# Kernel optimization log

Hardware: AMD Instinct MI355X
Metric: run time of the kernel (lower is better)

The kernel has to match this reference:

```python
import jax, jax.numpy as jnp
import numpy as np

B, N, D, S, CD = 8, 2048, 512, 256, 768
H, DH = 8, 64
INNER = H * DH          # 512
FF = 4 * D              # 2048 (GEGLU inner)
EPS = 1e-5


def setup_inputs() -> dict:
    key = jax.random.key(0)
    ks = jax.random.split(key, 24)
    w = lambda k, shp: (jax.random.normal(k, shp, dtype=jnp.float32) * 0.02)
    inp = {
        "x": jax.random.normal(ks[0], (B, N, D), dtype=jnp.float32),
        "context": jax.random.normal(ks[1], (B, S, CD), dtype=jnp.float32),
        "lengths": jax.random.randint(ks[2], (B,), 1, N + 1).astype(jnp.int32),
        # self-attention (attn1)
        "wq1": w(ks[3], (D, INNER)), "wk1": w(ks[4], (D, INNER)), "wv1": w(ks[5], (D, INNER)),
        "wo1": w(ks[6], (INNER, D)), "bo1": jnp.zeros((D,), jnp.float32),
        # cross-attention (attn2)
        "wq2": w(ks[7], (D, INNER)), "wk2": w(ks[8], (CD, INNER)), "wv2": w(ks[9], (CD, INNER)),
        "wo2": w(ks[10], (INNER, D)), "bo2": jnp.zeros((D,), jnp.float32),
        # GEGLU feed-forward
        "wff_in": w(ks[11], (D, 2 * FF)), "bff_in": jnp.zeros((2 * FF,), jnp.float32),
        "wff_out": w(ks[12], (FF, D)), "bff_out": jnp.zeros((D,), jnp.float32),
        # LayerNorms
        "g1": jnp.ones((D,), jnp.float32), "b1": jnp.zeros((D,), jnp.float32),
        "g2": jnp.ones((D,), jnp.float32), "b2": jnp.zeros((D,), jnp.float32),
        "g3": jnp.ones((D,), jnp.float32), "b3": jnp.zeros((D,), jnp.float32),
    }
    return inp


def _ln(t, g, b):
    m = jnp.mean(t, axis=-1, keepdims=True)
    v = jnp.mean(jnp.square(t - m), axis=-1, keepdims=True)
    return (t - m) * jax.lax.rsqrt(v + EPS) * g + b


def _mha(q, k, v, key_mask):
    # q: [B,Nq,INNER], k/v: [B,Nk,INNER], key_mask: [B,Nk] bool or None
    split = lambda t: t.reshape(t.shape[0], t.shape[1], H, DH).transpose(0, 2, 1, 3)
    qh, kh, vh = split(q), split(k), split(v)
    scores = jnp.einsum("bhqd,bhkd->bhqk", qh, kh) * (DH ** -0.5)
    if key_mask is not None:
        scores = jnp.where(key_mask[:, None, None, :], scores, -1e30)
    attn = jax.nn.softmax(scores, axis=-1)
    out = jnp.einsum("bhqk,bhkd->bhqd", attn, vh)
    return out.transpose(0, 2, 1, 3).reshape(q.shape[0], q.shape[1], INNER)


def reference(x, context, lengths, wq1, wk1, wv1, wo1, bo1,
              wq2, wk2, wv2, wo2, bo2,
              wff_in, bff_in, wff_out, bff_out,
              g1, b1, g2, b2, g3, b3):
    tok_mask = jnp.arange(N)[None, :] < lengths[:, None]  # [B,N] valid tokens
    # --- self-attention (attn1), pre-norm, jagged -> key-masked ---
    h = _ln(x, g1, b1)
    a = _mha(h @ wq1, h @ wk1, h @ wv1, tok_mask) @ wo1 + bo1
    x = x + a
    # --- cross-attention (attn2) to dense context ---
    h = _ln(x, g2, b2)
    a = _mha(h @ wq2, context @ wk2, context @ wv2, None) @ wo2 + bo2
    x = x + a
    # --- GEGLU feed-forward ---
    h = _ln(x, g3, b3)
    p = h @ wff_in + bff_in
    a, gate = jnp.split(p, 2, axis=-1)
    x = x + (a * jax.nn.gelu(gate, approximate=False)) @ wff_out + bff_out
    # zero out padded positions (they don't exist in the jagged tensor)
    return x * tok_mask[..., None].astype(x.dtype)
```

## Files before the change

kernel.cpp:

```cpp
#include <hip/hip_runtime.h>
#include <stdint.h>


typedef __bf16 bf16x8 __attribute__((ext_vector_type(8)));
typedef float f32x4 __attribute__((ext_vector_type(4)));

__device__ __forceinline__ unsigned short f2b(float f) {
  union { float f; unsigned u; } v; v.f = f;
  return (unsigned short)((v.u + 0x7FFFu + ((v.u >> 16) & 1u)) >> 16);
}
__device__ __forceinline__ float b2f(unsigned short s) {
  union { unsigned u; float f; } v; v.u = ((unsigned)s) << 16; return v.f;
}
__device__ __forceinline__ f32x4 mfma16(bf16x8 a, bf16x8 b, f32x4 c) {
  return __builtin_amdgcn_mfma_f32_16x16x32_bf16(a, b, c, 0, 0, 0);
}

__global__ __launch_bounds__(256) void wtrans(const float* __restrict__ in,
                                              unsigned short* __restrict__ out,
                                              int R, int C) {
  __shared__ unsigned short t[32][33];
  int tx = threadIdx.x & 31, ty = threadIdx.x >> 5;
  int c0 = blockIdx.x * 32, r0 = blockIdx.y * 32;
#pragma unroll
  for (int i = 0; i < 32; i += 8)
    t[ty + i][tx] = f2b(in[(size_t)(r0 + ty + i) * C + c0 + tx]);
  __syncthreads();
#pragma unroll
  for (int i = 0; i < 32; i += 8)
    out[(size_t)(c0 + ty + i) * R + r0 + tx] = t[tx][ty + i];
}

__global__ __launch_bounds__(256) void castbf(const float* __restrict__ in,
                                              unsigned short* __restrict__ out,
                                              int n4) {
  int i = blockIdx.x * 256 + threadIdx.x;
  if (i >= n4) return;
  float4 v = ((const float4*)in)[i];
  unsigned long long p = (unsigned long long)f2b(v.x) |
                         ((unsigned long long)f2b(v.y) << 16) |
                         ((unsigned long long)f2b(v.z) << 32) |
                         ((unsigned long long)f2b(v.w) << 48);
  ((unsigned long long*)out)[i] = p;
}

__global__ __launch_bounds__(256) void ln_rows(const float* __restrict__ x,
                                               const float* __restrict__ g,
                                               const float* __restrict__ bb,
                                               unsigned short* __restrict__ out) {
  int row = blockIdx.x * 4 + (threadIdx.x >> 6);
  int lane = threadIdx.x & 63;
  const float* xr = x + (size_t)row * 512 + lane * 8;
  float4 a = *(const float4*)xr;
  float4 c = *(const float4*)(xr + 4);
  float av[8] = {a.x, a.y, a.z, a.w, c.x, c.y, c.z, c.w};
  float s = 0.f, q = 0.f;
#pragma unroll
  for (int j = 0; j < 8; j++) { s += av[j]; q += av[j] * av[j]; }
#pragma unroll
  for (int d = 1; d < 64; d <<= 1) { s += __shfl_xor(s, d); q += __shfl_xor(q, d); }
  float mean = s * (1.f / 512.f);
  float var = q * (1.f / 512.f) - mean * mean;
  float rs = rsqrtf(var + 1e-5f);
  const float* gp = g + lane * 8;
  const float* bp = bb + lane * 8;
  unsigned rr[4];
#pragma unroll
  for (int j = 0; j < 4; j++) {
    float y0 = (av[2 * j] - mean) * rs * gp[2 * j] + bp[2 * j];
    float y1 = (av[2 * j + 1] - mean) * rs * gp[2 * j + 1] + bp[2 * j + 1];
    rr[j] = (unsigned)f2b(y0) | ((unsigned)f2b(y1) << 16);
  }
  *(uint4*)(out + (size_t)row * 512 + lane * 8) = make_uint4(rr[0], rr[1], rr[2], rr[3]);
}

template <int EPI>
__global__ __launch_bounds__(256) void gemm128(const unsigned short* __restrict__ A,
                                               const unsigned short* __restrict__ Bt,
                                               void* __restrict__ Cp,
                                               const float* __restrict__ bias,
                                               const float* __restrict__ res,
                                               int M, int N, int K) {
  __shared__ unsigned short As[128 * 32];
  __shared__ unsigned short Bs[128 * 32];
  int tid = threadIdx.x;
  int wave = tid >> 6, lane = tid & 63;
  int row0 = blockIdx.x * 128, col0 = blockIdx.y * 128;
  int wr = wave >> 1, wc = wave & 1;
  f32x4 acc[4][4] = {};
  int sr = tid >> 1, sk = (tid & 1) << 4;
  const unsigned short* gA = A + (size_t)(row0 + sr) * K + sk;
  const unsigned short* gB = Bt + (size_t)(col0 + sr) * K + sk;
  int l15 = lane & 15, l4 = (lane >> 4) << 3;
  int rA = (wr * 64 + l15) * 32 + l4;
  int rB = (wc * 64 + l15) * 32 + l4;
  for (int kt = 0; kt < K; kt += 32) {
    *(uint4*)&As[sr * 32 + sk] = *(const uint4*)(gA + kt);
    *(uint4*)&As[sr * 32 + sk + 8] = *(const uint4*)(gA + kt + 8);
    *(uint4*)&Bs[sr * 32 + sk] = *(const uint4*)(gB + kt);
    *(uint4*)&Bs[sr * 32 + sk + 8] = *(const uint4*)(gB + kt + 8);
    __syncthreads();
    bf16x8 af[4], bq[4];
#pragma unroll
    for (int m = 0; m < 4; m++) af[m] = *(const bf16x8*)&As[rA + m * 16 * 32];
#pragma unroll
    for (int n = 0; n < 4; n++) bq[n] = *(const bf16x8*)&Bs[rB + n * 16 * 32];
#pragma unroll
    for (int m = 0; m < 4; m++)
#pragma unroll
      for (int n = 0; n < 4; n++)
        acc[m][n] = mfma16(af[m], bq[n], acc[m][n]);
    __syncthreads();
  }
  int lr = (lane >> 4) * 4;
#pragma unroll
  for (int m = 0; m < 4; m++)
#pragma unroll
    for (int n = 0; n < 4; n++)
#pragma unroll
      for (int r = 0; r < 4; r++) {
        int grow = row0 + wr * 64 + m * 16 + lr + r;
        int gcol = col0 + wc * 64 + n * 16 + l15;
        size_t gi = (size_t)grow * N + gcol;
        float v = acc[m][n][r];
        if (EPI == 0) {
          ((unsigned short*)Cp)[gi] = f2b(v);
        } else if (EPI == 1) {
          ((unsigned short*)Cp)[gi] = f2b(v + bias[gcol]);
        } else {
          ((float*)Cp)[gi] = v + bias[gcol] + res[gi];
        }
      }
}

__global__ __launch_bounds__(256) void attn(const unsigned short* __restrict__ Q,
                                            const unsigned short* __restrict__ Kg,
                                            const unsigned short* __restrict__ Vg,
                                            unsigned short* __restrict__ O,
                                            const int* __restrict__ lengths,
                                            int nq, int nkv, int maskkv) {
  int qblk = blockIdx.x, h = blockIdx.y, b = blockIdx.z;
  int tid = threadIdx.x, wave = tid >> 6, lane = tid & 63;
  int len = lengths[b];
  int qbase = qblk * 64;
  if (qbase >= len) return;
  int kvlen = maskkv ? len : nkv;
  int nt = (kvlen + 31) >> 5;

  __shared__ unsigned short Ks[32][72];
  __shared__ unsigned short Vf[2048];
  __shared__ unsigned short Ps[4][16][40];

  int l15 = lane & 15, lh = lane >> 4, l4 = lh * 8;
  const unsigned short* qp =
      Q + (size_t)(b * nq + qbase + wave * 16 + l15) * 512 + h * 64 + l4;
  bf16x8 aq0 = *(const bf16x8*)qp;
  bf16x8 aq1 = *(const bf16x8*)(qp + 32);
  const unsigned short* kgp = Kg + (size_t)b * nkv * 512 + h * 64;
  const unsigned short* vgp = Vg + (size_t)b * nkv * 512 + h * 64;

  f32x4 oacc[4] = {};
  float m_r[4], l_r[4];
#pragma unroll
  for (int r = 0; r < 4; r++) { m_r[r] = -3e38f; l_r[r] = 0.f; }

  int skey = tid >> 3, sd0 = (tid & 7) * 8;
  int vdh = tid & 63, vkg = tid >> 6;

  for (int t = 0; t < nt; t++) {
    int kv0 = t * 32;
    *(uint4*)&Ks[skey][sd0] =
        *(const uint4*)(kgp + (size_t)(kv0 + skey) * 512 + sd0);
    {
      unsigned short tmp[8];
#pragma unroll
      for (int kj = 0; kj < 8; kj++)
        tmp[kj] = vgp[(size_t)(kv0 + vkg * 8 + kj) * 512 + vdh];
      unsigned w0 = (unsigned)tmp[0] | ((unsigned)tmp[1] << 16);
      unsigned w1 = (unsigned)tmp[2] | ((unsigned)tmp[3] << 16);
      unsigned w2 = (unsigned)tmp[4] | ((unsigned)tmp[5] << 16);
      unsigned w3 = (unsigned)tmp[6] | ((unsigned)tmp[7] << 16);
      *(uint4*)&Vf[(vkg * 64 + vdh) * 8] = make_uint4(w0, w1, w2, w3);
    }
    __syncthreads();

    f32x4 sf[2];
#pragma unroll
    for (int c = 0; c < 2; c++) {
      bf16x8 bk0 = *(const bf16x8*)&Ks[c * 16 + l15][l4];
      bf16x8 bk1 = *(const bf16x8*)&Ks[c * 16 + l15][32 + l4];
      f32x4 z = {};
      z = mfma16(aq0, bk0, z);
      z = mfma16(aq1, bk1, z);
      sf[c] = z;
    }
#pragma unroll
    for (int c = 0; c < 2; c++) {
      bool kval = (kv0 + c * 16 + l15) < kvlen;
#pragma unroll
      for (int r = 0; r < 4; r++)
        sf[c][r] = kval ? sf[c][r] * 0.125f : -1e30f;
    }
    float mt[4], ps[4];
#pragma unroll
    for (int r = 0; r < 4; r++) mt[r] = fmaxf(sf[0][r], sf[1][r]);
#pragma unroll
    for (int d = 1; d < 16; d <<= 1)
#pragma unroll
      for (int r = 0; r < 4; r++) mt[r] = fmaxf(mt[r], __shfl_xor(mt[r], d));
    float sc[4];
#pragma unroll
    for (int r = 0; r < 4; r++) {
      float mn = fmaxf(m_r[r], mt[r]);
      sc[r] = __expf(m_r[r] - mn);
      m_r[r] = mn;
      ps[r] = 0.f;
    }
#pragma unroll
    for (int c = 0; c < 2; c++)
#pragma unroll
      for (int r = 0; r < 4; r++) {
        float pe = __expf(sf[c][r] - m_r[r]);
        ps[r] += pe;
        Ps[wave][lh * 4 + r][c * 16 + l15] = f2b(pe);
      }
#pragma unroll
    for (int d = 1; d < 16; d <<= 1)
#pragma unroll
      for (int r = 0; r < 4; r++) ps[r] += __shfl_xor(ps[r], d);
#pragma unroll
    for (int r = 0; r < 4; r++) l_r[r] = l_r[r] * sc[r] + ps[r];
#pragma unroll
    for (int nf = 0; nf < 4; nf++)
#pragma unroll
      for (int r = 0; r < 4; r++) oacc[nf][r] *= sc[r];
    bf16x8 pf = *(const bf16x8*)&Ps[wave][l15][l4];
#pragma unroll
    for (int nf = 0; nf < 4; nf++) {
      bf16x8 vf = *(const bf16x8*)&Vf[(lh * 64 + nf * 16 + l15) * 8];
      oacc[nf] = mfma16(pf, vf, oacc[nf]);
    }
    __syncthreads();
  }
#pragma unroll
  for (int nf = 0; nf < 4; nf++)
#pragma unroll
    for (int r = 0; r < 4; r++) {
      float ov = oacc[nf][r] / l_r[r];
      int qrow = qbase + wave * 16 + lh * 4 + r;
      O[(size_t)(b * nq + qrow) * 512 + h * 64 + nf * 16 + l15] = f2b(ov);
    }
}

__global__ __launch_bounds__(256) void geglu(const unsigned short* __restrict__ p,
                                             unsigned short* __restrict__ out) {
  int idx = blockIdx.x * 256 + threadIdx.x;
  int row = idx >> 8, c = (idx & 255) << 3;
  const unsigned short* pr = p + (size_t)row * 4096 + c;
  uint4 av = *(const uint4*)pr;
  uint4 gv = *(const uint4*)(pr + 2048);
  const unsigned short* ap = (const unsigned short*)&av;
  const unsigned short* gp = (const unsigned short*)&gv;
  unsigned rr[4];
#pragma unroll
  for (int j = 0; j < 4; j++) {
    float a0 = b2f(ap[2 * j]), a1 = b2f(ap[2 * j + 1]);
    float x0 = b2f(gp[2 * j]), x1 = b2f(gp[2 * j + 1]);
    float y0 = a0 * 0.5f * x0 * (1.f + erff(x0 * 0.70710678118f));
    float y1 = a1 * 0.5f * x1 * (1.f + erff(x1 * 0.70710678118f));
    rr[j] = (unsigned)f2b(y0) | ((unsigned)f2b(y1) << 16);
  }
  *(uint4*)(out + (size_t)row * 2048 + c) = make_uint4(rr[0], rr[1], rr[2], rr[3]);
}

__global__ __launch_bounds__(256) void maskout_f32(const float* __restrict__ xb,
                                                   const int* __restrict__ lengths,
                                                   float* __restrict__ out) {
  int idx = blockIdx.x * 256 + threadIdx.x;
  int row = idx >> 6, c = (idx & 63) << 3;
  int b = row >> 11, n = row & 2047;
  bool val = n < lengths[b];
  float4 v0 = make_float4(0.f, 0.f, 0.f, 0.f), v1 = v0;
  if (val) {
    const float* xr = xb + (size_t)row * 512 + c;
    v0 = *(const float4*)xr;
    v1 = *(const float4*)(xr + 4);
  }
  float* orp = out + (size_t)row * 512 + c;
  *(float4*)orp = v0;
  *(float4*)(orp + 4) = v1;
}

extern "C" void kernel_launch(void* const* d_in, const int* in_sizes, int n_in,
                              void* d_out, int out_size, void* d_ws, size_t ws_size,
                              hipStream_t stream) {
  const float* x = (const float*)d_in[0];
  const float* ctx = (const float*)d_in[1];
  const int* lengths = (const int*)d_in[2];
  const float* wq1 = (const float*)d_in[3];
  const float* wk1 = (const float*)d_in[4];
  const float* wv1 = (const float*)d_in[5];
  const float* wo1 = (const float*)d_in[6];
  const float* bo1 = (const float*)d_in[7];
  const float* wq2 = (const float*)d_in[8];
  const float* wk2 = (const float*)d_in[9];
  const float* wv2 = (const float*)d_in[10];
  const float* wo2 = (const float*)d_in[11];
  const float* bo2 = (const float*)d_in[12];
  const float* wffin = (const float*)d_in[13];
  const float* bffin = (const float*)d_in[14];
  const float* wffout = (const float*)d_in[15];
  const float* bffout = (const float*)d_in[16];
  const float* g1 = (const float*)d_in[17];
  const float* b1 = (const float*)d_in[18];
  const float* g2 = (const float*)d_in[19];
  const float* b2 = (const float*)d_in[20];
  const float* g3 = (const float*)d_in[21];
  const float* b3 = (const float*)d_in[22];

  char* ws = (char*)d_ws;
  size_t o = 0;
  auto alloc = [&](size_t bytes) {
    size_t r = o;
    o += (bytes + 255) & ~(size_t)255;
    return r;
  };
  unsigned short* WQ1T = (unsigned short*)(ws + alloc(512 * 512 * 2));
  unsigned short* WK1T = (unsigned short*)(ws + alloc(512 * 512 * 2));
  unsigned short* WV1T = (unsigned short*)(ws + alloc(512 * 512 * 2));
  unsigned short* WO1T = (unsigned short*)(ws + alloc(512 * 512 * 2));
  unsigned short* WQ2T = (unsigned short*)(ws + alloc(512 * 512 * 2));
  unsigned short* WK2T = (unsigned short*)(ws + alloc(512 * 768 * 2));
  unsigned short* WV2T = (unsigned short*)(ws + alloc(512 * 768 * 2));
  unsigned short* WO2T = (unsigned short*)(ws + alloc(512 * 512 * 2));
  unsigned short* WFFINT = (unsigned short*)(ws + alloc(4096 * 512 * 2));
  unsigned short* WFFOUTT = (unsigned short*)(ws + alloc(512 * 2048 * 2));
  float* XBUF = (float*)(ws + alloc((size_t)16384 * 512 * 4));
  unsigned short* HB = (unsigned short*)(ws + alloc((size_t)16384 * 512 * 2));
  unsigned short* QB = (unsigned short*)(ws + alloc((size_t)16384 * 512 * 2));
  unsigned short* KB = (unsigned short*)(ws + alloc((size_t)16384 * 512 * 2));
  unsigned short* VB = (unsigned short*)(ws + alloc((size_t)16384 * 512 * 2));
  unsigned short* AO = (unsigned short*)(ws + alloc((size_t)16384 * 512 * 2));
  unsigned short* CTXB = KB;
  unsigned short* K2B = KB + (size_t)4 * 1024 * 1024 / 2;
  unsigned short* V2B = KB + (size_t)8 * 1024 * 1024 / 2;
  unsigned short* PCH = QB;
  unsigned short* GCH = VB;

  wtrans<<<dim3(16, 16), 256, 0, stream>>>(wq1, WQ1T, 512, 512);
  wtrans<<<dim3(16, 16), 256, 0, stream>>>(wk1, WK1T, 512, 512);
  wtrans<<<dim3(16, 16), 256, 0, stream>>>(wv1, WV1T, 512, 512);
  wtrans<<<dim3(16, 16), 256, 0, stream>>>(wo1, WO1T, 512, 512);
  wtrans<<<dim3(16, 16), 256, 0, stream>>>(wq2, WQ2T, 512, 512);
  wtrans<<<dim3(16, 24), 256, 0, stream>>>(wk2, WK2T, 768, 512);
  wtrans<<<dim3(16, 24), 256, 0, stream>>>(wv2, WV2T, 768, 512);
  wtrans<<<dim3(16, 16), 256, 0, stream>>>(wo2, WO2T, 512, 512);
  wtrans<<<dim3(128, 16), 256, 0, stream>>>(wffin, WFFINT, 512, 4096);
  wtrans<<<dim3(16, 64), 256, 0, stream>>>(wffout, WFFOUTT, 2048, 512);

  ln_rows<<<4096, 256, 0, stream>>>(x, g1, b1, HB);
  gemm128<0><<<dim3(128, 4), 256, 0, stream>>>(HB, WQ1T, QB, nullptr, nullptr, 16384, 512, 512);
  gemm128<0><<<dim3(128, 4), 256, 0, stream>>>(HB, WK1T, KB, nullptr, nullptr, 16384, 512, 512);
  gemm128<0><<<dim3(128, 4), 256, 0, stream>>>(HB, WV1T, VB, nullptr, nullptr, 16384, 512, 512);
  attn<<<dim3(32, 8, 8), 256, 0, stream>>>(QB, KB, VB, AO, lengths, 2048, 2048, 1);
  gemm128<2><<<dim3(128, 4), 256, 0, stream>>>(AO, WO1T, XBUF, bo1, x, 16384, 512, 512);

  ln_rows<<<4096, 256, 0, stream>>>(XBUF, g2, b2, HB);
  castbf<<<1536, 256, 0, stream>>>(ctx, CTXB, 2048 * 768 / 4);
  gemm128<0><<<dim3(128, 4), 256, 0, stream>>>(HB, WQ2T, QB, nullptr, nullptr, 16384, 512, 512);
  gemm128<0><<<dim3(16, 4), 256, 0, stream>>>(CTXB, WK2T, K2B, nullptr, nullptr, 2048, 512, 768);
  gemm128<0><<<dim3(16, 4), 256, 0, stream>>>(CTXB, WV2T, V2B, nullptr, nullptr, 2048, 512, 768);
  attn<<<dim3(32, 8, 8), 256, 0, stream>>>(QB, K2B, V2B, AO, lengths, 2048, 256, 0);
  gemm128<2><<<dim3(128, 4), 256, 0, stream>>>(AO, WO2T, XBUF, bo2, XBUF, 16384, 512, 512);

  ln_rows<<<4096, 256, 0, stream>>>(XBUF, g3, b3, HB);
  for (int ch = 0; ch < 4; ch++) {
    const unsigned short* hc = HB + (size_t)ch * 4096 * 512;
    float* xc = XBUF + (size_t)ch * 4096 * 512;
    gemm128<1><<<dim3(32, 32), 256, 0, stream>>>(hc, WFFINT, PCH, bffin, nullptr, 4096, 4096, 512);
    geglu<<<4096, 256, 0, stream>>>(PCH, GCH);
    gemm128<2><<<dim3(32, 4), 256, 0, stream>>>(GCH, WFFOUTT, xc, bffout, xc, 4096, 512, 2048);
  }

  maskout_f32<<<4096, 256, 0, stream>>>(XBUF, lengths, (float*)d_out);
}
```

Measured before the change: 938.8 us.

## Stage GEMM tiles via direct global-to-LDS loads and fuse final masking

GEMM tile staging now uses global_load_lds so data goes straight from global memory into shared memory without passing through registers, with a new wave-based row/column mapping. The final token mask is applied in a new epilogue of the FF-out GEMM, which writes directly to the output and removes the separate maskout kernel. The risks are correct synchronization of the asynchronous LDS loads and the loss of register-level prefetch control.

```diff
diff --git a/kernel.cpp b/kernel.cpp
--- a/kernel.cpp
+++ b/kernel.cpp
@@ -14,6 +14,11 @@
 }
 __device__ __forceinline__ f32x4 mfma16(bf16x8 a, bf16x8 b, f32x4 c) {
   return __builtin_amdgcn_mfma_f32_16x16x32_bf16(a, b, c, 0, 0, 0);
+}
+__device__ __forceinline__ void gload16(const void* g, void* l) {
+  __builtin_amdgcn_global_load_lds((const __attribute__((address_space(1))) void*)g,
+                                   (__attribute__((address_space(3))) void*)l,
+                                   16, 0, 0);
 }
 
 __global__ __launch_bounds__(256) void wtrans(const float* __restrict__ in,
@@ -80,6 +85,7 @@
                                                void* __restrict__ Cp,
                                                const float* __restrict__ bias,
                                                const float* __restrict__ res,
+                                               const int* __restrict__ lens,
                                                int M, int N, int K) {
   __shared__ unsigned short As[128 * 32];
   __shared__ unsigned short Bs[128 * 32];
@@ -88,17 +94,22 @@
   int row0 = blockIdx.x * 128, col0 = blockIdx.y * 128;
   int wr = wave >> 1, wc = wave & 1;
   f32x4 acc[4][4] = {};
-  int sr = tid >> 1, sk = (tid & 1) << 4;
-  const unsigned short* gA = A + (size_t)(row0 + sr) * K + sk;
-  const unsigned short* gB = Bt + (size_t)(col0 + sr) * K + sk;
+  int srow = wave * 32 + (lane >> 2);
+  int scol = (lane & 3) * 8;
+  const unsigned short* gA0 = A + (size_t)(row0 + srow) * K + scol;
+  const unsigned short* gB0 = Bt + (size_t)(col0 + srow) * K + scol;
+  unsigned short* lA0 = &As[(wave * 32) * 32];
+  unsigned short* lA1 = &As[(wave * 32 + 16) * 32];
+  unsigned short* lB0 = &Bs[(wave * 32) * 32];
+  unsigned short* lB1 = &Bs[(wave * 32 + 16) * 32];
   int l15 = lane & 15, l4 = (lane >> 4) << 3;
   int rA = (wr * 64 + l15) * 32 + l4;
   int rB = (wc * 64 + l15) * 32 + l4;
   for (int kt = 0; kt < K; kt += 32) {
-    *(uint4*)&As[sr * 32 + sk] = *(const uint4*)(gA + kt);
-    *(uint4*)&As[sr * 32 + sk + 8] = *(const uint4*)(gA + kt + 8);
-    *(uint4*)&Bs[sr * 32 + sk] = *(const uint4*)(gB + kt);
-    *(uint4*)&Bs[sr * 32 + sk + 8] = *(const uint4*)(gB + kt + 8);
+    gload16(gA0 + kt, lA0);
+    gload16(gA0 + (size_t)16 * K + kt, lA1);
+    gload16(gB0 + kt, lB0);
+    gload16(gB0 + (size_t)16 * K + kt, lB1);
     __syncthreads();
     bf16x8 af[4], bq[4];
 #pragma unroll
@@ -127,8 +138,11 @@
           ((unsigned short*)Cp)[gi] = f2b(v);
         } else if (EPI == 1) {
           ((unsigned short*)Cp)[gi] = f2b(v + bias[gcol]);
+        } else if (EPI == 2) {
+          ((float*)Cp)[gi] = v + bias[gcol] + res[gi];
         } else {
-          ((float*)Cp)[gi] = v + bias[gcol] + res[gi];
+          int bb = grow >> 11, nn = grow & 2047;
+          ((float*)Cp)[gi] = (nn < lens[bb]) ? (v + bias[gcol] + res[gi]) : 0.f;
         }
       }
 }
@@ -271,24 +285,6 @@
     rr[j] = (unsigned)f2b(y0) | ((unsigned)f2b(y1) << 16);
   }
   *(uint4*)(out + (size_t)row * 2048 + c) = make_uint4(rr[0], rr[1], rr[2], rr[3]);
-}
-
-__global__ __launch_bounds__(256) void maskout_f32(const float* __restrict__ xb,
-                                                   const int* __restrict__ lengths,
-                                                   float* __restrict__ out) {
-  int idx = blockIdx.x * 256 + threadIdx.x;
-  int row = idx >> 6, c = (idx & 63) << 3;
-  int b = row >> 11, n = row & 2047;
-  bool val = n < lengths[b];
-  float4 v0 = make_float4(0.f, 0.f, 0.f, 0.f), v1 = v0;
-  if (val) {
-    const float* xr = xb + (size_t)row * 512 + c;
-    v0 = *(const float4*)xr;
-    v1 = *(const float4*)(xr + 4);
-  }
-  float* orp = out + (size_t)row * 512 + c;
-  *(float4*)orp = v0;
-  *(float4*)(orp + 4) = v1;
 }
 
 extern "C" void kernel_launch(void* const* d_in, const int* in_sizes, int n_in,
@@ -359,28 +355,27 @@
   wtrans<<<dim3(16, 64), 256, 0, stream>>>(wffout, WFFOUTT, 2048, 512);
 
   ln_rows<<<4096, 256, 0, stream>>>(x, g1, b1, HB);
-  gemm128<0><<<dim3(128, 4), 256, 0, stream>>>(HB, WQ1T, QB, nullptr, nullptr, 16384, 512, 512);
-  gemm128<0><<<dim3(128, 4), 256, 0, stream>>>(HB, WK1T, KB, nullptr, nullptr, 16384, 512, 512);
-  gemm128<0><<<dim3(128, 4), 256, 0, stream>>>(HB, WV1T, VB, nullptr, nullptr, 16384, 512, 512);
+  gemm128<0><<<dim3(128, 4), 256, 0, stream>>>(HB, WQ1T, QB, nullptr, nullptr, nullptr, 16384, 512, 512);
+  gemm128<0><<<dim3(128, 4), 256, 0, stream>>>(HB, WK1T, KB, nullptr, nullptr, nullptr, 16384, 512, 512);
+  gemm128<0><<<dim3(128, 4), 256, 0, stream>>>(HB, WV1T, VB, nullptr, nullptr, nullptr, 16384, 512, 512);
   attn<<<dim3(32, 8, 8), 256, 0, stream>>>(QB, KB, VB, AO, lengths, 2048, 2048, 1);
-  gemm128<2><<<dim3(128, 4), 256, 0, stream>>>(AO, WO1T, XBUF, bo1, x, 16384, 512, 512);
+  gemm128<2><<<dim3(128, 4), 256, 0, stream>>>(AO, WO1T, XBUF, bo1, x, nullptr, 16384, 512, 512);
 
   ln_rows<<<4096, 256, 0, stream>>>(XBUF, g2, b2, HB);
   castbf<<<1536, 256, 0, stream>>>(ctx, CTXB, 2048 * 768 / 4);
-  gemm128<0><<<dim3(128, 4), 256, 0, stream>>>(HB, WQ2T, QB, nullptr, nullptr, 16384, 512, 512);
-  gemm128<0><<<dim3(16, 4), 256, 0, stream>>>(CTXB, WK2T, K2B, nullptr, nullptr, 2048, 512, 768);
-  gemm128<0><<<dim3(16, 4), 256, 0, stream>>>(CTXB, WV2T, V2B, nullptr, nullptr, 2048, 512, 768);
+  gemm128<0><<<dim3(128, 4), 256, 0, stream>>>(HB, WQ2T, QB, nullptr, nullptr, nullptr, 16384, 512, 512);
+  gemm128<0><<<dim3(16, 4), 256, 0, stream>>>(CTXB, WK2T, K2B, nullptr, nullptr, nullptr, 2048, 512, 768);
+  gemm128<0><<<dim3(16, 4), 256, 0, stream>>>(CTXB, WV2T, V2B, nullptr, nullptr, nullptr, 2048, 512, 768);
   attn<<<dim3(32, 8, 8), 256, 0, stream>>>(QB, K2B, V2B, AO, lengths, 2048, 256, 0);
-  gemm128<2><<<dim3(128, 4), 256, 0, stream>>>(AO, WO2T, XBUF, bo2, XBUF, 16384, 512, 512);
+  gemm128<2><<<dim3(128, 4), 256, 0, stream>>>(AO, WO2T, XBUF, bo2, XBUF, nullptr, 16384, 512, 512);
 
   ln_rows<<<4096, 256, 0, stream>>>(XBUF, g3, b3, HB);
   for (int ch = 0; ch < 4; ch++) {
     const unsigned short* hc = HB + (size_t)ch * 4096 * 512;
     float* xc = XBUF + (size_t)ch * 4096 * 512;
-    gemm128<1><<<dim3(32, 32), 256, 0, stream>>>(hc, WFFINT, PCH, bffin, nullptr, 4096, 4096, 512);
+    float* oc = (float*)d_out + (size_t)ch * 4096 * 512;
+    gemm128<1><<<dim3(32, 32), 256, 0, stream>>>(hc, WFFINT, PCH, bffin, nullptr, nullptr, 4096, 4096, 512);
     geglu<<<4096, 256, 0, stream>>>(PCH, GCH);
-    gemm128<2><<<dim3(32, 4), 256, 0, stream>>>(GCH, WFFOUTT, xc, bffout, xc, 4096, 512, 2048);
-  }
-
-  maskout_f32<<<4096, 256, 0, stream>>>(XBUF, lengths, (float*)d_out);
-}
+    gemm128<3><<<dim3(32, 4), 256, 0, stream>>>(GCH, WFFOUTT, oc, bffout, xc, lengths + ch * 2, 4096, 512, 2048);
+  }
+}
```

Measured after the change: 924.1 us. Within noise of the previous version (-1.6%).
